# Kernel tuning notes

Hardware: AMD Instinct MI355X
Metric: run time of the kernel (lower is better)

The kernel has to match this reference:

```python
import jax, jax.numpy as jnp
import numpy as np

N_QUBITS = 8
EMBED_DIM = 1024
FFN_DIM = 4096


def setup_inputs() -> dict:
    key = jax.random.key(0)
    ks = jax.random.split(key, 6)
    x = jax.random.normal(ks[0], (8, 4096, EMBED_DIM), dtype=jnp.float32)
    # trainable RY rotation angles, one per wire (torchquantum RY has_params=True)
    theta = jax.random.normal(ks[1], (N_QUBITS,), dtype=jnp.float32)
    # torch nn.Linear params: W [out, in], b [out]
    W1 = jax.random.normal(ks[2], (FFN_DIM, N_QUBITS), dtype=jnp.float32) / np.sqrt(N_QUBITS)
    b1 = jnp.zeros((FFN_DIM,), dtype=jnp.float32)
    W2 = jax.random.normal(ks[3], (EMBED_DIM, FFN_DIM), dtype=jnp.float32) / np.sqrt(FFN_DIM)
    b2 = jnp.zeros((EMBED_DIM,), dtype=jnp.float32)
    return {"x": x, "theta": theta, "W1": W1, "b1": b1, "W2": W2, "b2": b2}


def reference(x, theta, W1, b1, W2, b2):
    # Quantum layer: per token, encoder resets state to |0..0>, applies RX(x_i)
    # on wire i, then trainable RY(theta_i), then measures <Z_i>. The circuit has
    # no entangling gates, so it factorizes per wire with the closed form:
    #   <Z_i> = cos(theta_i) * cos(x[..., i])
    # (RY(t)RX(a)|0> gives <Z> = cos t * cos a). Vectorized over batch and seq.
    q = jnp.cos(theta) * jnp.cos(x[..., :N_QUBITS])   # [B, S, n_qubits]
    # dropout is identity in eval mode
    h = jax.nn.relu(jnp.einsum('bsq,fq->bsf', q, W1) + b1)  # [B, S, ffn]
    out = jnp.einsum('bsf,ef->bse', h, W2) + b2              # [B, S, embed]
    return out
```

## Files before the change

### kernel.cpp

```cpp
#include <hip/hip_runtime.h>
#include <cstdint>
#include <cstddef>


#define M_TOT 32768L
#define N_DIM 1024
#define K_DIM 4096
#define BM 256
#define BN 256
#define BK 64
#define NT_K (K_DIM / BK)
#define CM_MAX 16384L

typedef __attribute__((ext_vector_type(8))) short short8;
typedef __attribute__((ext_vector_type(4))) float f32x4;

__device__ __forceinline__ uint16_t f2bf(float f) {
  uint32_t u = __builtin_bit_cast(uint32_t, f);
  uint32_t r = (u + 0x7fffu + ((u >> 16) & 1u)) >> 16;
  return (uint16_t)r;
}

__device__ __forceinline__ void gload_lds16(const void* gsrc, void* ldst) {
  __builtin_amdgcn_global_load_lds(
      (const __attribute__((address_space(1))) void*)gsrc,
      (__attribute__((address_space(3))) void*)ldst, 16, 0, 0);
}

__global__ __launch_bounds__(256) void prep_w2(const float* __restrict__ W2,
                                               uint16_t* __restrict__ W2sw) {
  long idx = (long)blockIdx.x * 256 + threadIdx.x;
  long e8 = idx * 8;
  int e = (int)(e8 >> 12);
  int k = (int)(e8 & 4095);
  float4 v0 = *(const float4*)(W2 + e8);
  float4 v1 = *(const float4*)(W2 + e8 + 4);
  union { uint16_t u[8]; uint4 v; } pk;
  pk.u[0] = f2bf(v0.x); pk.u[1] = f2bf(v0.y); pk.u[2] = f2bf(v0.z); pk.u[3] = f2bf(v0.w);
  pk.u[4] = f2bf(v1.x); pk.u[5] = f2bf(v1.y); pk.u[6] = f2bf(v1.z); pk.u[7] = f2bf(v1.w);
  int sg = ((k >> 3) & 7) ^ (e & 7);
  uint16_t* dst = W2sw + (long)e * 4096 + (k & ~63) + sg * 8;
  *(uint4*)dst = pk.v;
}

__global__ __launch_bounds__(256) void h_kernel(const float* __restrict__ x,
                                                const float* __restrict__ theta,
                                                const float* __restrict__ W1,
                                                const float* __restrict__ b1,
                                                uint16_t* __restrict__ Hsw) {
  __shared__ float qs[32][8];
  int tid = threadIdx.x;
  long m0 = (long)blockIdx.x * 32;
  int g = blockIdx.y * 256 + tid;
  int f0 = g * 8;

  {
    int t = tid >> 3, i = tid & 7;
    qs[t][i] = __cosf(theta[i]) * cosf(x[(m0 + t) * 1024 + i]);
  }
  __syncthreads();

  float4 w[16];
#pragma unroll
  for (int j = 0; j < 8; ++j) {
    w[2 * j]     = *(const float4*)(W1 + (long)(f0 + j) * 8);
    w[2 * j + 1] = *(const float4*)(W1 + (long)(f0 + j) * 8 + 4);
  }
  float bb[8];
#pragma unroll
  for (int j = 0; j < 8; ++j) bb[j] = b1[f0 + j];

  int blk = (g >> 3) * 64;
  int gw = g & 7;

#pragma unroll 4
  for (int t = 0; t < 32; ++t) {
    long m = m0 + t;
    float q0 = qs[t][0], q1 = qs[t][1], q2 = qs[t][2], q3 = qs[t][3];
    float q4 = qs[t][4], q5 = qs[t][5], q6 = qs[t][6], q7 = qs[t][7];
    union { uint16_t u[8]; uint4 v; } pk;
#pragma unroll
    for (int j = 0; j < 8; ++j) {
      float h = bb[j];
      h += q0 * w[2 * j].x + q1 * w[2 * j].y + q2 * w[2 * j].z + q3 * w[2 * j].w;
      h += q4 * w[2 * j + 1].x + q5 * w[2 * j + 1].y + q6 * w[2 * j + 1].z + q7 * w[2 * j + 1].w;
      h = fmaxf(h, 0.0f);
      pk.u[j] = f2bf(h);
    }
    int sg = gw ^ ((int)m & 7);
    *(uint4*)&Hsw[m * K_DIM + blk + sg * 8] = pk.v;
  }
}

__global__ __launch_bounds__(512, 2) void gemm_kernel(const uint16_t* __restrict__ Hsw,
                                                      const uint16_t* __restrict__ W2sw,
                                                      const float* __restrict__ b2,
                                                      float* __restrict__ out) {
  __shared__ uint16_t LA[2 * BM * BK];
  __shared__ uint16_t LB[2 * BN * BK];

  int nwg = gridDim.x;
  int bid = blockIdx.x;
  int sw = bid;
  if ((nwg & 7) == 0) { int cpx = nwg >> 3; sw = (bid & 7) * cpx + (bid >> 3); }
  const int NTN = N_DIM / BN;
  int mt = sw / NTN;
  int nt = sw - mt * NTN;
  long m0 = (long)mt * BM;
  int n0 = nt * BN;

  int tid = threadIdx.x;
  int lane = tid & 63;
  int wave_m = (tid >> 6) >> 2;
  int wave_n = (tid >> 6) & 3;
  int wmB = wave_m * 128;
  int wnB = wave_n * 64;

  int r  = lane & 15;
  int kq = lane >> 4;
  int xr = r & 7;

  int rowS = tid >> 3;
  int colS = (tid & 7) * 8;
  const uint16_t* srcA = Hsw  + (m0 + rowS) * K_DIM + colS;
  const uint16_t* srcB = W2sw + ((long)(n0 + rowS)) * K_DIM + colS;
  int ldsWB = (tid & ~63) * 8;

#define STAGE_A(p, h, j, t) \
  gload_lds16(srcA + (long)((h)*128 + (j)*64) * K_DIM + (t)*BK, \
              &LA[(p)*16384 + ((h)*128 + (j)*64)*BK + ldsWB])
#define STAGE_B(p, h, j, t) \
  gload_lds16(srcB + (long)((h)*128 + (j)*64) * K_DIM + (t)*BK, \
              &LB[(p)*16384 + ((h)*128 + (j)*64)*BK + ldsWB])

#define BAR() do { asm volatile("" ::: "memory"); __builtin_amdgcn_s_barrier(); \
                   asm volatile("" ::: "memory"); } while (0)
#define SGB(m_, n_) __builtin_amdgcn_sched_group_barrier((m_), (n_), 0)

#define LDA_F(p, mf_, ks_) \
  (*(const short8*)&LA[(p)*16384 + (wmB + (mf_)*16 + r)*BK + ((((ks_)*4 + kq) ^ xr)*8)])
#define LDB_F(p, nf_, ks_) \
  (*(const short8*)&LB[(p)*16384 + (wnB + (nf_)*16 + r)*BK + ((((ks_)*4 + kq) ^ xr)*8)])

#define MFMA_Q(AARR, BARR, mh, nh) do { \
    _Pragma("unroll") for (int i_ = 0; i_ < 4; ++i_) \
    _Pragma("unroll") for (int j_ = 0; j_ < 2; ++j_) \
    _Pragma("unroll") for (int ks_ = 0; ks_ < 2; ++ks_) \
      acc[(mh)*4 + i_][(nh)*2 + j_] = __builtin_amdgcn_mfma_f32_16x16x32_bf16( \
          AARR[i_][ks_], BARR[j_][ks_], acc[(mh)*4 + i_][(nh)*2 + j_], 0, 0, 0); \
  } while (0)

#define READ_B1V(p) do { \
    _Pragma("unroll") for (int j_ = 0; j_ < 2; ++j_) \
    _Pragma("unroll") for (int ks_ = 0; ks_ < 2; ++ks_) \
      b1v[j_][ks_] = LDB_F(p, 2 + j_, ks_); \
  } while (0)
#define READ_A1(p) do { \
    _Pragma("unroll") for (int i_ = 0; i_ < 4; ++i_) \
    _Pragma("unroll") for (int ks_ = 0; ks_ < 2; ++ks_) \
      a1[i_][ks_] = LDA_F(p, 4 + i_, ks_); \
  } while (0)
#define READ_A0(pn) do { \
    _Pragma("unroll") for (int i_ = 0; i_ < 4; ++i_) \
    _Pragma("unroll") for (int ks_ = 0; ks_ < 2; ++ks_) \
      a0[i_][ks_] = LDA_F(pn, i_, ks_); \
  } while (0)
#define READ_B0(pn) do { \
    _Pragma("unroll") for (int j_ = 0; j_ < 2; ++j_) \
    _Pragma("unroll") for (int ks_ = 0; ks_ < 2; ++ks_) \
      b0[j_][ks_] = LDB_F(pn, j_, ks_); \
  } while (0)

  f32x4 acc[8][4];
#pragma unroll
  for (int i = 0; i < 8; ++i)
#pragma unroll
    for (int j = 0; j < 4; ++j) acc[i][j] = (f32x4){0.f, 0.f, 0.f, 0.f};

  short8 a0[4][2];
  short8 a1[4][2];
  short8 b0[2][2];
  short8 b1v[2][2];

#pragma unroll
  for (int h = 0; h < 2; ++h)
#pragma unroll
    for (int j = 0; j < 2; ++j) STAGE_A(0, h, j, 0);
#pragma unroll
  for (int h = 0; h < 2; ++h)
#pragma unroll
    for (int j = 0; j < 2; ++j) STAGE_B(0, h, j, 0);
#pragma unroll
  for (int h = 0; h < 2; ++h)
#pragma unroll
    for (int j = 0; j < 2; ++j) STAGE_A(1, h, j, 1);
#pragma unroll
  for (int h = 0; h < 2; ++h)
#pragma unroll
    for (int j = 0; j < 2; ++j) STAGE_B(1, h, j, 1);
  asm volatile("s_waitcnt vmcnt(8)" ::: "memory");
  BAR();
  READ_A0(0);
  READ_B0(0);

#pragma unroll 2
  for (int u = 0; u < NT_K; ++u) {
    int p = u & 1;
    int tc = (u + 2 < NT_K) ? (u + 2) : (NT_K - 1);

    MFMA_Q(a0, b0, 0, 0);
    READ_B1V(p);
    READ_A1(p);
#pragma unroll
    for (int s_ = 0; s_ < 12; ++s_) { SGB(0x8, 1); SGB(0x100, 1); }
    SGB(0x8, 4);
    BAR();

    STAGE_A(p, 0, 0, tc); STAGE_A(p, 1, 0, tc);
    MFMA_Q(a0, b1v, 0, 1);
    SGB(0x10, 1); SGB(0x8, 8); SGB(0x10, 1); SGB(0x8, 8);
    BAR();

    STAGE_B(p, 0, 0, tc); STAGE_B(p, 0, 1, tc);
    STAGE_B(p, 1, 0, tc); STAGE_B(p, 1, 1, tc);
    MFMA_Q(a1, b1v, 1, 1);
#pragma unroll
    for (int s_ = 0; s_ < 4; ++s_) { SGB(0x10, 1); SGB(0x8, 4); }
    asm volatile("s_waitcnt vmcnt(6)" ::: "memory");
    BAR();

    READ_A0(p ^ 1);
    MFMA_Q(a1, b0, 1, 0);
    READ_B0(p ^ 1);
    STAGE_A(p, 0, 1, tc); STAGE_A(p, 1, 1, tc);
#pragma unroll
    for (int s_ = 0; s_ < 8; ++s_) { SGB(0x8, 1); SGB(0x100, 1); }
    SGB(0x10, 2); SGB(0x8, 8); SGB(0x100, 4);
    BAR();
  }

  float bb[4];
#pragma unroll
  for (int nf = 0; nf < 4; ++nf) bb[nf] = b2[n0 + wnB + nf * 16 + r];
  long mbase = m0 + wmB + kq * 4;
#pragma unroll
  for (int mf = 0; mf < 8; ++mf) {
#pragma unroll
    for (int nf = 0; nf < 4; ++nf) {
      int n = n0 + wnB + nf * 16 + r;
#pragma unroll
      for (int rg = 0; rg < 4; ++rg) {
        out[(mbase + mf * 16 + rg) * N_DIM + n] = acc[mf][nf][rg] + bb[nf];
      }
    }
  }
#undef STAGE_A
#undef STAGE_B
#undef BAR
#undef SGB
#undef LDA_F
#undef LDB_F
#undef MFMA_Q
#undef READ_B1V
#undef READ_A1
#undef READ_A0
#undef READ_B0
}

extern "C" void kernel_launch(void* const* d_in, const int* in_sizes, int n_in,
                              void* d_out, int out_size, void* d_ws, size_t ws_size,
                              hipStream_t stream) {
  const float* x     = (const float*)d_in[0];
  const float* theta = (const float*)d_in[1];
  const float* W1    = (const float*)d_in[2];
  const float* b1    = (const float*)d_in[3];
  const float* W2    = (const float*)d_in[4];
  const float* b2    = (const float*)d_in[5];
  float* out = (float*)d_out;

  const size_t W2SW_BYTES = (size_t)N_DIM * K_DIM * 2;
  uint16_t* W2sw = (uint16_t*)d_ws;
  uint16_t* Hsw  = (uint16_t*)((char*)d_ws + W2SW_BYTES);

  size_t avail = ws_size > W2SW_BYTES ? ws_size - W2SW_BYTES : 0;
  long CM = (long)(avail / ((size_t)K_DIM * 2));
  CM &= ~255L;
  if (CM > CM_MAX) CM = CM_MAX;
  if (CM < 256) CM = 256;

  prep_w2<<<2048, 256, 0, stream>>>(W2, W2sw);

  for (long m0 = 0; m0 < M_TOT; m0 += CM) {
    long mc = M_TOT - m0;
    if (mc > CM) mc = CM;
    dim3 gA((unsigned)(mc / 32), 2);
    h_kernel<<<gA, 256, 0, stream>>>(x + m0 * N_DIM, theta, W1, b1, Hsw);
    unsigned ngb = (unsigned)((mc / BM) * (N_DIM / BN));
    gemm_kernel<<<ngb, 512, 0, stream>>>(Hsw, W2sw, b2, out + m0 * N_DIM);
  }
}
```

Before: 297.0 us.

## Fuse hidden-layer computation into GEMM, generating H tiles in LDS on the fly

Removes the separate h_kernel and its materialized bf16 H buffer in global memory. Each GEMM workgroup now computes q = cos(theta)*cos(x) for its 256 rows, then recomputes relu(q·W1+b1) per K-tile with fp16 dot2 instructions and writes it swizzled into LDS as the A operand. W1/b1 are prepacked to fp16 slices that are streamed with global_load_lds, and the MFMA/schedule pipeline is restructured around this. This avoids writing and re-reading the large H tensor and the chunked launches. The cost is extra VALU work inside the GEMM main loop, since each H tile is recomputed by all four N-tile workgroups. q and W1 are also rounded to fp16 before the dot product, which can change accuracy.

Result: slower. 515.2 us (+73.5%).

```diff
diff --git a/kernel.cpp b/kernel.cpp
--- a/kernel.cpp
+++ b/kernel.cpp
@@ -10,10 +10,12 @@
 #define BN 256
 #define BK 64
 #define NT_K (K_DIM / BK)
-#define CM_MAX 16384L
+#define W1SL 1536L
 
 typedef __attribute__((ext_vector_type(8))) short short8;
 typedef __attribute__((ext_vector_type(4))) float f32x4;
+typedef __attribute__((ext_vector_type(8))) _Float16 half8v;
+typedef __attribute__((ext_vector_type(2))) _Float16 h2;
 
 __device__ __forceinline__ uint16_t f2bf(float f) {
   uint32_t u = __builtin_bit_cast(uint32_t, f);
@@ -21,10 +23,12 @@
   return (uint16_t)r;
 }
 
-__device__ __forceinline__ void gload_lds16(const void* gsrc, void* ldst) {
-  __builtin_amdgcn_global_load_lds(
-      (const __attribute__((address_space(1))) void*)gsrc,
-      (__attribute__((address_space(3))) void*)ldst, 16, 0, 0);
+__device__ __forceinline__ float dot8(half8v q, half8v w, float c) {
+  c = __builtin_amdgcn_fdot2((h2){q[0], q[1]}, (h2){w[0], w[1]}, c, false);
+  c = __builtin_amdgcn_fdot2((h2){q[2], q[3]}, (h2){w[2], w[3]}, c, false);
+  c = __builtin_amdgcn_fdot2((h2){q[4], q[5]}, (h2){w[4], w[5]}, c, false);
+  c = __builtin_amdgcn_fdot2((h2){q[6], q[7]}, (h2){w[6], w[7]}, c, false);
+  return c;
 }
 
 __global__ __launch_bounds__(256) void prep_w2(const float* __restrict__ W2,
@@ -43,66 +47,36 @@
   *(uint4*)dst = pk.v;
 }
 
-__global__ __launch_bounds__(256) void h_kernel(const float* __restrict__ x,
-                                                const float* __restrict__ theta,
-                                                const float* __restrict__ W1,
-                                                const float* __restrict__ b1,
-                                                uint16_t* __restrict__ Hsw) {
-  __shared__ float qs[32][8];
+__global__ __launch_bounds__(256) void prep_w1hb(const float* __restrict__ W1,
+                                                 const float* __restrict__ b1,
+                                                 char* __restrict__ W1HB) {
+  int t = blockIdx.x;
   int tid = threadIdx.x;
-  long m0 = (long)blockIdx.x * 32;
-  int g = blockIdx.y * 256 + tid;
-  int f0 = g * 8;
-
-  {
-    int t = tid >> 3, i = tid & 7;
-    qs[t][i] = __cosf(theta[i]) * cosf(x[(m0 + t) * 1024 + i]);
+  int f = tid >> 2;
+  int pr = tid & 3;
+  const float* src = W1 + ((long)t * 64 + f) * 8 + pr * 2;
+  h2 v = {(_Float16)src[0], (_Float16)src[1]};
+  *(h2*)(W1HB + (long)t * W1SL + (f + (f >> 3)) * 16 + pr * 4) = v;
+  if (tid < 64) {
+    *(float*)(W1HB + (long)t * W1SL + 1152 + tid * 4) = b1[t * 64 + tid];
   }
-  __syncthreads();
-
-  float4 w[16];
-#pragma unroll
-  for (int j = 0; j < 8; ++j) {
-    w[2 * j]     = *(const float4*)(W1 + (long)(f0 + j) * 8);
-    w[2 * j + 1] = *(const float4*)(W1 + (long)(f0 + j) * 8 + 4);
-  }
-  float bb[8];
-#pragma unroll
-  for (int j = 0; j < 8; ++j) bb[j] = b1[f0 + j];
-
-  int blk = (g >> 3) * 64;
-  int gw = g & 7;
-
-#pragma unroll 4
-  for (int t = 0; t < 32; ++t) {
-    long m = m0 + t;
-    float q0 = qs[t][0], q1 = qs[t][1], q2 = qs[t][2], q3 = qs[t][3];
-    float q4 = qs[t][4], q5 = qs[t][5], q6 = qs[t][6], q7 = qs[t][7];
-    union { uint16_t u[8]; uint4 v; } pk;
-#pragma unroll
-    for (int j = 0; j < 8; ++j) {
-      float h = bb[j];
-      h += q0 * w[2 * j].x + q1 * w[2 * j].y + q2 * w[2 * j].z + q3 * w[2 * j].w;
-      h += q4 * w[2 * j + 1].x + q5 * w[2 * j + 1].y + q6 * w[2 * j + 1].z + q7 * w[2 * j + 1].w;
-      h = fmaxf(h, 0.0f);
-      pk.u[j] = f2bf(h);
-    }
-    int sg = gw ^ ((int)m & 7);
-    *(uint4*)&Hsw[m * K_DIM + blk + sg * 8] = pk.v;
-  }
-}
-
-__global__ __launch_bounds__(512, 2) void gemm_kernel(const uint16_t* __restrict__ Hsw,
+}
+
+__global__ __launch_bounds__(512, 2) void gemm_kernel(const float* __restrict__ x,
+                                                      const float* __restrict__ theta,
                                                       const uint16_t* __restrict__ W2sw,
+                                                      const char* __restrict__ W1HB,
                                                       const float* __restrict__ b2,
                                                       float* __restrict__ out) {
   __shared__ uint16_t LA[2 * BM * BK];
   __shared__ uint16_t LB[2 * BN * BK];
+  __shared__ __align__(16) _Float16 qsh[256][8];
+  __shared__ __align__(16) char W1S[2][2048];
 
   int nwg = gridDim.x;
   int bid = blockIdx.x;
-  int sw = bid;
-  if ((nwg & 7) == 0) { int cpx = nwg >> 3; sw = (bid & 7) * cpx + (bid >> 3); }
+  int cpx = nwg >> 3;
+  int sw = (bid & 7) * cpx + (bid >> 3);
   const int NTN = N_DIM / BN;
   int mt = sw / NTN;
   int nt = sw - mt * NTN;
@@ -121,21 +95,26 @@
   int xr = r & 7;
 
   int rowS = tid >> 3;
-  int colS = (tid & 7) * 8;
-  const uint16_t* srcA = Hsw  + (m0 + rowS) * K_DIM + colS;
-  const uint16_t* srcB = W2sw + ((long)(n0 + rowS)) * K_DIM + colS;
+  int gw   = tid & 7;
+  const uint16_t* srcB = W2sw + ((long)(n0 + rowS)) * K_DIM + gw * 8;
   int ldsWB = (tid & ~63) * 8;
 
-#define STAGE_A(p, h, j, t) \
-  gload_lds16(srcA + (long)((h)*128 + (j)*64) * K_DIM + (t)*BK, \
-              &LA[(p)*16384 + ((h)*128 + (j)*64)*BK + ldsWB])
 #define STAGE_B(p, h, j, t) \
-  gload_lds16(srcB + (long)((h)*128 + (j)*64) * K_DIM + (t)*BK, \
-              &LB[(p)*16384 + ((h)*128 + (j)*64)*BK + ldsWB])
+  __builtin_amdgcn_global_load_lds( \
+      (const __attribute__((address_space(1))) void*)(srcB + (long)((h)*128 + (j)*64) * K_DIM + (t)*BK), \
+      (__attribute__((address_space(3))) void*)&LB[(p)*16384 + ((h)*128 + (j)*64)*BK + ldsWB], 16, 0, 0)
+
+#define STAGE_W1(tcl, bi) \
+  __builtin_amdgcn_global_load_lds( \
+      (const __attribute__((address_space(1))) void*)(W1HB + (long)(tcl)*W1SL + tid*4), \
+      (__attribute__((address_space(3))) void*)&W1S[bi][(tid & ~63)*4], 4, 0, 0)
 
 #define BAR() do { asm volatile("" ::: "memory"); __builtin_amdgcn_s_barrier(); \
                    asm volatile("" ::: "memory"); } while (0)
 #define SGB(m_, n_) __builtin_amdgcn_sched_group_barrier((m_), (n_), 0)
+#define SB0() __builtin_amdgcn_sched_barrier(0)
+#define LGKM0() asm volatile("s_waitcnt lgkmcnt(0)" ::: "memory")
+#define VMC(n_) asm volatile("s_waitcnt vmcnt(" #n_ ")" ::: "memory")
 
 #define LDA_F(p, mf_, ks_) \
   (*(const short8*)&LA[(p)*16384 + (wmB + (mf_)*16 + r)*BK + ((((ks_)*4 + kq) ^ xr)*8)])
@@ -150,25 +129,47 @@
           AARR[i_][ks_], BARR[j_][ks_], acc[(mh)*4 + i_][(nh)*2 + j_], 0, 0, 0); \
   } while (0)
 
-#define READ_B1V(p) do { \
-    _Pragma("unroll") for (int j_ = 0; j_ < 2; ++j_) \
-    _Pragma("unroll") for (int ks_ = 0; ks_ < 2; ++ks_) \
-      b1v[j_][ks_] = LDB_F(p, 2 + j_, ks_); \
+#define READ_A0(p) do { \
+    _Pragma("unroll") for (int i_ = 0; i_ < 4; ++i_) \
+    _Pragma("unroll") for (int ks_ = 0; ks_ < 2; ++ks_) \
+      a0[i_][ks_] = LDA_F(p, i_, ks_); \
   } while (0)
 #define READ_A1(p) do { \
     _Pragma("unroll") for (int i_ = 0; i_ < 4; ++i_) \
     _Pragma("unroll") for (int ks_ = 0; ks_ < 2; ++ks_) \
       a1[i_][ks_] = LDA_F(p, 4 + i_, ks_); \
   } while (0)
-#define READ_A0(pn) do { \
-    _Pragma("unroll") for (int i_ = 0; i_ < 4; ++i_) \
-    _Pragma("unroll") for (int ks_ = 0; ks_ < 2; ++ks_) \
-      a0[i_][ks_] = LDA_F(pn, i_, ks_); \
-  } while (0)
 #define READ_B0(pn) do { \
     _Pragma("unroll") for (int j_ = 0; j_ < 2; ++j_) \
     _Pragma("unroll") for (int ks_ = 0; ks_ < 2; ++ks_) \
       b0[j_][ks_] = LDB_F(pn, j_, ks_); \
+  } while (0)
+#define READ_B1V(pn) do { \
+    _Pragma("unroll") for (int j_ = 0; j_ < 2; ++j_) \
+    _Pragma("unroll") for (int ks_ = 0; ks_ < 2; ++ks_) \
+      b1v[j_][ks_] = LDB_F(pn, 2 + j_, ks_); \
+  } while (0)
+
+#define CSTAGE_A(pdst, bufr_, h, j) do { \
+    int row_l = (h)*128 + (j)*64 + rowS; \
+    half8v qv = *(const half8v*)&qsh[row_l][0]; \
+    const _Float16* W1f_ = (const _Float16*)W1S[bufr_]; \
+    union { uint16_t u[8]; uint4 v; } pk_; \
+    _Pragma("unroll") for (int jj = 0; jj < 8; ++jj) { \
+      half8v wv = *(const half8v*)&W1f_[(gw * 9 + jj) * 8]; \
+      float hs = dot8(qv, wv, bb1[jj]); \
+      pk_.u[jj] = f2bf(fmaxf(hs, 0.0f)); \
+    } \
+    *(uint4*)&LA[(pdst)*16384 + row_l*BK + ((gw ^ (row_l & 7))*8)] = pk_.v; \
+  } while (0)
+
+#define CSTAGE_ALL(pdst, bufr_) do { \
+    const float* b1sf_ = (const float*)(W1S[bufr_] + 1152); \
+    float4 bA_ = *(const float4*)&b1sf_[gw * 8]; \
+    float4 bB_ = *(const float4*)&b1sf_[gw * 8 + 4]; \
+    float bb1[8] = {bA_.x, bA_.y, bA_.z, bA_.w, bB_.x, bB_.y, bB_.z, bB_.w}; \
+    CSTAGE_A(pdst, bufr_, 0, 0); CSTAGE_A(pdst, bufr_, 1, 0); \
+    CSTAGE_A(pdst, bufr_, 0, 1); CSTAGE_A(pdst, bufr_, 1, 1); \
   } while (0)
 
   f32x4 acc[8][4];
@@ -182,62 +183,75 @@
   short8 b0[2][2];
   short8 b1v[2][2];
 
-#pragma unroll
-  for (int h = 0; h < 2; ++h)
-#pragma unroll
-    for (int j = 0; j < 2; ++j) STAGE_A(0, h, j, 0);
-#pragma unroll
-  for (int h = 0; h < 2; ++h)
-#pragma unroll
-    for (int j = 0; j < 2; ++j) STAGE_B(0, h, j, 0);
-#pragma unroll
-  for (int h = 0; h < 2; ++h)
-#pragma unroll
-    for (int j = 0; j < 2; ++j) STAGE_A(1, h, j, 1);
-#pragma unroll
-  for (int h = 0; h < 2; ++h)
-#pragma unroll
-    for (int j = 0; j < 2; ++j) STAGE_B(1, h, j, 1);
-  asm volatile("s_waitcnt vmcnt(8)" ::: "memory");
+  {
+    int t2 = tid >> 1, hf = tid & 1;
+    float4 xv = *(const float4*)(x + (m0 + t2) * 1024 + hf * 4);
+    float4 th = *(const float4*)(theta + hf * 4);
+    union { _Float16 h[4]; short4 s; } qp;
+    qp.h[0] = (_Float16)(__cosf(th.x) * cosf(xv.x));
+    qp.h[1] = (_Float16)(__cosf(th.y) * cosf(xv.y));
+    qp.h[2] = (_Float16)(__cosf(th.z) * cosf(xv.z));
+    qp.h[3] = (_Float16)(__cosf(th.w) * cosf(xv.w));
+    *(short4*)&qsh[t2][hf * 4] = qp.s;
+  }
+  __syncthreads();
+
+  STAGE_W1(0, 0);
+  SB0();
+  STAGE_B(0, 0, 0, 0); STAGE_B(0, 0, 1, 0); STAGE_B(0, 1, 0, 0); STAGE_B(0, 1, 1, 0);
+  SB0();
+  STAGE_W1(1, 1);
+  SB0();
+  STAGE_B(1, 0, 0, 1); STAGE_B(1, 0, 1, 1); STAGE_B(1, 1, 0, 1); STAGE_B(1, 1, 1, 1);
+  VMC(9);
   BAR();
-  READ_A0(0);
+  CSTAGE_ALL(0, 0);
+  LGKM0();
+  VMC(5);
+  BAR();
   READ_B0(0);
+  READ_B1V(0);
 
 #pragma unroll 2
   for (int u = 0; u < NT_K; ++u) {
     int p = u & 1;
     int tc = (u + 2 < NT_K) ? (u + 2) : (NT_K - 1);
 
+    READ_A0(p);
     MFMA_Q(a0, b0, 0, 0);
-    READ_B1V(p);
+    MFMA_Q(a0, b1v, 0, 1);
     READ_A1(p);
-#pragma unroll
-    for (int s_ = 0; s_ < 12; ++s_) { SGB(0x8, 1); SGB(0x100, 1); }
-    SGB(0x8, 4);
+    STAGE_W1(tc, p);
+    SGB(0x100, 8);
+    SGB(0x10, 1);
+#pragma unroll
+    for (int s_ = 0; s_ < 8; ++s_) { SGB(0x8, 4); SGB(0x100, 1); }
+    VMC(5);
+    LGKM0();
     BAR();
 
-    STAGE_A(p, 0, 0, tc); STAGE_A(p, 1, 0, tc);
-    MFMA_Q(a0, b1v, 0, 1);
-    SGB(0x10, 1); SGB(0x8, 8); SGB(0x10, 1); SGB(0x8, 8);
-    BAR();
-
+    CSTAGE_ALL(p ^ 1, p ^ 1);
+    MFMA_Q(a1, b1v, 1, 1);
     STAGE_B(p, 0, 0, tc); STAGE_B(p, 0, 1, tc);
     STAGE_B(p, 1, 0, tc); STAGE_B(p, 1, 1, tc);
-    MFMA_Q(a1, b1v, 1, 1);
-#pragma unroll
-    for (int s_ = 0; s_ < 4; ++s_) { SGB(0x10, 1); SGB(0x8, 4); }
-    asm volatile("s_waitcnt vmcnt(6)" ::: "memory");
+    SGB(0x10, 4);
+#pragma unroll
+    for (int s_ = 0; s_ < 16; ++s_) { SGB(0x100, 2); SGB(0x2, 12); SGB(0x8, 1); }
+    SGB(0x200, 4);
+    VMC(5);
+    LGKM0();
     BAR();
 
-    READ_A0(p ^ 1);
     MFMA_Q(a1, b0, 1, 0);
     READ_B0(p ^ 1);
-    STAGE_A(p, 0, 1, tc); STAGE_A(p, 1, 1, tc);
-#pragma unroll
-    for (int s_ = 0; s_ < 8; ++s_) { SGB(0x8, 1); SGB(0x100, 1); }
-    SGB(0x10, 2); SGB(0x8, 8); SGB(0x100, 4);
+    READ_B1V(p ^ 1);
+#pragma unroll
+    for (int s_ = 0; s_ < 6; ++s_) { SGB(0x8, 2); SGB(0x100, 2); }
+    SGB(0x8, 4);
+    LGKM0();
     BAR();
   }
+  VMC(0);
 
   float bb[4];
 #pragma unroll
@@ -254,17 +268,22 @@
       }
     }
   }
-#undef STAGE_A
 #undef STAGE_B
+#undef STAGE_W1
 #undef BAR
 #undef SGB
+#undef SB0
+#undef LGKM0
+#undef VMC
 #undef LDA_F
 #undef LDB_F
 #undef MFMA_Q
+#undef READ_A0
+#undef READ_A1
+#undef READ_B0
 #undef READ_B1V
-#undef READ_A1
-#undef READ_A0
-#undef READ_B0
+#undef CSTAGE_A
+#undef CSTAGE_ALL
 }
 
 extern "C" void kernel_launch(void* const* d_in, const int* in_sizes, int n_in,
@@ -280,22 +299,11 @@
 
   const size_t W2SW_BYTES = (size_t)N_DIM * K_DIM * 2;
   uint16_t* W2sw = (uint16_t*)d_ws;
-  uint16_t* Hsw  = (uint16_t*)((char*)d_ws + W2SW_BYTES);
-
-  size_t avail = ws_size > W2SW_BYTES ? ws_size - W2SW_BYTES : 0;
-  long CM = (long)(avail / ((size_t)K_DIM * 2));
-  CM &= ~255L;
-  if (CM > CM_MAX) CM = CM_MAX;
-  if (CM < 256) CM = 256;
+  char* W1HB = (char*)d_ws + W2SW_BYTES;
 
   prep_w2<<<2048, 256, 0, stream>>>(W2, W2sw);
-
-  for (long m0 = 0; m0 < M_TOT; m0 += CM) {
-    long mc = M_TOT - m0;
-    if (mc > CM) mc = CM;
-    dim3 gA((unsigned)(mc / 32), 2);
-    h_kernel<<<gA, 256, 0, stream>>>(x + m0 * N_DIM, theta, W1, b1, Hsw);
-    unsigned ngb = (unsigned)((mc / BM) * (N_DIM / BN));
-    gemm_kernel<<<ngb, 512, 0, stream>>>(Hsw, W2sw, b2, out + m0 * N_DIM);
-  }
-}
+  prep_w1hb<<<64, 256, 0, stream>>>(W1, b1, W1HB);
+
+  unsigned ngb = (unsigned)((M_TOT / BM) * (N_DIM / BN));
+  gemm_kernel<<<ngb, 512, 0, stream>>>(x, theta, W2sw, W1HB, b2, out);
+}
```
